# Kernel optimization log

Measured on AMD Instinct MI355X. Metric: run time of the kernel, lower is better.

Reference implementation:

```python
import jax, jax.numpy as jnp
import numpy as np

GROUPS = 2
STRIDE = (1, 1)
PADDING = ((1, 1), (1, 1))
DILATION = (1, 1)


def setup_inputs() -> dict:
    key = jax.random.key(0)
    k1, k2, k3 = jax.random.split(key, 3)
    B, Cin, H, W = 16, 256, 112, 112
    Cout, kH, kW = 256, 3, 3
    x = jax.random.normal(k1, (B, Cin, H, W), dtype=jnp.float32)
    # kaiming_uniform-like scale: fan_in = (Cin/groups)*kH*kW
    fan_in = (Cin // GROUPS) * kH * kW
    bound = float(np.sqrt(1.0 / fan_in))
    weight = jax.random.uniform(k2, (Cout, Cin // GROUPS, kH, kW), dtype=jnp.float32,
                                minval=-bound, maxval=bound)
    bias = jax.random.uniform(k3, (Cout,), dtype=jnp.float32, minval=-bound, maxval=bound)
    return {"x": x, "weight": weight, "bias": bias}


def reference(x, weight, bias):
    # Grouped conv2d: every backend path of SparseGroupedConv2d (sparse triton
    # active-tile kernel, zero-tile skip, dense F.conv2d fallback) computes this
    # exact grouped convolution; the tile machinery only skips zero-energy tiles.
    y = jax.lax.conv_general_dilated(
        x, weight,
        window_strides=STRIDE,
        padding=PADDING,
        rhs_dilation=DILATION,
        dimension_numbers=("NCHW", "OIHW", "NCHW"),
        feature_group_count=GROUPS,
    )
    return y + bias[None, :, None, None]
```

## Files before the change

### kernel.cpp

```cpp
#include <hip/hip_runtime.h>
#include <hip/hip_bf16.h>
#include <stdint.h>

#define BATCH 16
#define CIN   256
#define HH    112
#define WW    112
#define GROUPS 2
#define CG    128
#define COG   128
#define CK    32

typedef __bf16 bf16x8 __attribute__((ext_vector_type(8)));
typedef float  f32x4  __attribute__((ext_vector_type(4)));

#define WB_BYTES   (GROUPS*3*3*COG*CG*2)
#define ZBUF_OFF   WB_BYTES
#define ZBUF_BYTES 8192
#define XB_OFF     (ZBUF_OFF + ZBUF_BYTES)
#define XB_BYTES   ((size_t)BATCH*HH*WW*CIN*2)
#define WS_NEED    ((size_t)XB_OFF + XB_BYTES)

__device__ inline void load_lds16(const void* g, void* l) {
    __builtin_amdgcn_global_load_lds(
        (const __attribute__((address_space(1))) void*)g,
        (__attribute__((address_space(3))) void*)l, 16, 0, 0);
}

__global__ __launch_bounds__(256) void k_wcvt(const float* __restrict__ w,
                                              ushort* __restrict__ wb) {
    int i = blockIdx.x * 256 + threadIdx.x;
    int ci = i & 127;
    int t  = i >> 7;
    int co = t & 127;
    t >>= 7;
    int kw = t % 3; t /= 3;
    int kh = t % 3;
    int g  = t / 3;
    int src = (((g*COG + co)*CG + ci)*3 + kh)*3 + kw;
    __hip_bfloat16 v = __float2bfloat16(w[src]);
    wb[i] = *reinterpret_cast<ushort*>(&v);
}

#define XPAD 113
__global__ __launch_bounds__(256) void k_xcvt(const float* __restrict__ x,
                                              ushort* __restrict__ xb) {
    __shared__ float tile[64 * XPAD];
    int bid = blockIdx.x;
    int cc  = bid & 3;
    int h   = (bid >> 2) % HH;
    int b   = bid / (4 * HH);
    int tid = threadIdx.x;

    const float* src = x + ((size_t)(b*CIN + cc*64) * HH + h) * WW;
    for (int tt = tid; tt < 64*28; tt += 256) {
        int c = tt / 28, v = tt % 28;
        float4 f = *reinterpret_cast<const float4*>(src + (size_t)c*HH*WW + v*4);
        float* d = &tile[c*XPAD + v*4];
        d[0]=f.x; d[1]=f.y; d[2]=f.z; d[3]=f.w;
    }
    __syncthreads();

    if (tid < 224) {
        int w = tid >> 1, half = tid & 1;
        ushort o[32];
#pragma unroll
        for (int j = 0; j < 32; ++j) {
            __hip_bfloat16 v = __float2bfloat16(tile[(half*32 + j)*XPAD + w]);
            o[j] = *reinterpret_cast<ushort*>(&v);
        }
        ushort* dst = xb + (((size_t)(b*HH + h)*WW + w)*CIN + cc*64 + half*32);
        const uint4* o4 = reinterpret_cast<const uint4*>(o);
        uint4* d4 = reinterpret_cast<uint4*>(dst);
        d4[0]=o4[0]; d4[1]=o4[1]; d4[2]=o4[2]; d4[3]=o4[3];
    }
}

__device__ inline void stage_w3(const ushort* __restrict__ wb, ushort* dstbuf,
                                int g, int tap_base, int cin, int wave, int lane) {
    int co = wave*16 + (lane >> 2);
    int ts = (lane & 3) ^ ((lane >> 3) & 3);
#pragma unroll
    for (int i = 0; i < 3; ++i) {
        const ushort* src = wb + (((size_t)(g*9 + tap_base + i)*COG + co)*CG + cin + ts*8);
        load_lds16(src, dstbuf + (i*COG + wave*16)*CK);
    }
}

__device__ inline void xpre48(const ushort* __restrict__ xb, ushort* dstbuf,
                              ushort* dump, const ushort* __restrict__ zbuf,
                              int b, int g, int oh0, int cin, int t, int lane,
                              bool real) {
    if (real && t < 42) {
        int rr = t / 7, ii = t % 7;
        int h  = oh0 - 1 + rr;
        int qv = lane >> 2;
        int w_in = ii*16 + qv;
        int ts = (lane & 3) ^ (((2*rr + 1 + qv) >> 1) & 3);
        const ushort* src = (h >= 0 && h < HH)
            ? xb + (((size_t)(b*HH + h)*WW + w_in)*CIN + g*CG + cin + ts*8)
            : zbuf + lane*8;
        load_lds16(src, dstbuf + (rr*114 + 1 + ii*16)*CK);
    } else {
        load_lds16(zbuf + lane*8, dump);
    }
}

#define WAITV(N) asm volatile("s_waitcnt vmcnt(" #N ")" ::: "memory");

#define TAPX(KH, KW, NT, NC)                                                \
  {                                                                         \
    int sB = lk ^ (((2*(wr + (KH)) + l15 + (KW)) >> 1) & 3);                \
    const ushort* bbase = xcur + ((wr + (KH))*114 + l15 + (KW))*CK + sB*8;  \
    bf16x8 xf[7];                                                           \
    _Pragma("unroll")                                                       \
    for (int i = 0; i < 7; ++i)                                             \
      xf[i] = *reinterpret_cast<const bf16x8*>(bbase + i*16*CK);            \
    const ushort* abase = wcur + ((KW)*COG + wm*64 + l15)*CK + sA*8;        \
    bf16x8 wf[4];                                                           \
    _Pragma("unroll")                                                       \
    for (int u = 0; u < 4; ++u)                                             \
      wf[u] = *reinterpret_cast<const bf16x8*>(abase + u*16*CK);            \
    if ((KW) == 0) stage_w3(wb, wnxt, g, (NT), (NC), wave, lane);           \
    if ((KW) <= 1)                                                          \
      xpre48(xb, xnxt, dump, zbuf, b, g, oh0, cinN,                         \
             wave + 8*((KH)*2 + (KW)), lane, c < 3);                        \
    __builtin_amdgcn_s_barrier();                                           \
    __builtin_amdgcn_s_setprio(1);                                          \
    _Pragma("unroll")                                                       \
    for (int u = 0; u < 4; ++u)                                             \
      _Pragma("unroll")                                                     \
      for (int i = 0; i < 7; ++i)                                           \
        acc[i][u] = __builtin_amdgcn_mfma_f32_16x16x32_bf16(                \
            xf[i], wf[u], acc[i][u], 0, 0, 0);                              \
    __builtin_amdgcn_s_setprio(0);                                          \
    if ((KW) == 2) { if ((KH) == 2) { WAITV(0) } else { WAITV(2) } }        \
    __builtin_amdgcn_s_barrier();                                           \
  }

#define GROUPSEC(KH, NT, NC) TAPX(KH,0,NT,NC) TAPX(KH,1,NT,NC) TAPX(KH,2,NT,NC)

__global__ __launch_bounds__(512, 2) void k_conv(const ushort* __restrict__ xb,
                                                 const ushort* __restrict__ wb,
                                                 const float* __restrict__ bias,
                                                 float* __restrict__ out,
                                                 const ushort* __restrict__ zbuf) {
    __shared__ __align__(16) ushort xs[2][6*114*CK];
    __shared__ __align__(16) ushort wsb[2][3*COG*CK];
    __shared__ __align__(16) ushort dump[512];

    int orig = (blockIdx.x & 7) * 112 + (blockIdx.x >> 3);
    int g   = orig / 448;
    int r   = orig % 448;
    int b   = r / 28;
    int q   = r % 28;
    int oh0 = q * 4;

    int tid  = threadIdx.x;
    int wave = tid >> 6;
    int lane = tid & 63;
    int wm   = wave >> 2;
    int wr   = wave & 3;
    int l15  = lane & 15;
    int lk   = lane >> 4;
    int sA   = lk ^ ((l15 >> 1) & 3);

    for (int t = tid; t < 768; t += 512) {
        int buf = t / 384, r2 = t % 384;
        int rr = r2 / 64, wc = (r2 >> 5) & 1, ch = r2 & 31;
        xs[buf][(rr*114 + wc*113)*CK + ch] = 0;
    }

    float bvreg[4];
#pragma unroll
    for (int u = 0; u < 4; ++u)
        bvreg[u] = bias[g*COG + wm*64 + u*16 + l15];

    f32x4 acc[7][4];
#pragma unroll
    for (int i = 0; i < 7; ++i)
#pragma unroll
        for (int u = 0; u < 4; ++u) acc[i][u] = f32x4{0.f,0.f,0.f,0.f};

    for (int k2 = 0; k2 < 6; ++k2)
        xpre48(xb, xs[0], dump, zbuf, b, g, oh0, 0, wave + 8*k2, lane, true);
    stage_w3(wb, wsb[0], g, 0, 0, wave, lane);
    WAITV(0)
    __builtin_amdgcn_s_barrier();

#pragma unroll 1
    for (int c = 0; c < 4; ++c) {
        const ushort* xcur = xs[c & 1];
        ushort* xnxt = xs[(c & 1) ^ 1];
        int cin  = c * CK;
        int cinN = ((c + 1) & 3) * CK;
        (void)cin;

        {
            const ushort* wcur = wsb[c & 1];
            ushort* wnxt = wsb[(c & 1) ^ 1];
            GROUPSEC(0, 3, c*CK)
        }
        {
            const ushort* wcur = wsb[(c + 1) & 1];
            ushort* wnxt = wsb[c & 1];
            GROUPSEC(1, 6, c*CK)
        }
        {
            const ushort* wcur = wsb[c & 1];
            ushort* wnxt = wsb[(c + 1) & 1];
            GROUPSEC(2, 0, cinN)
        }
    }

    int oh = oh0 + wr;
#pragma unroll
    for (int u = 0; u < 4; ++u) {
        int co = g*COG + wm*64 + u*16 + l15;
        float bv = bvreg[u];
        float* obase = out + (((size_t)(b*CIN + co)*HH + oh)*WW + lk*4);
#pragma unroll
        for (int i = 0; i < 7; ++i) {
            f32x4 v;
            v[0] = acc[i][u][0] + bv;
            v[1] = acc[i][u][1] + bv;
            v[2] = acc[i][u][2] + bv;
            v[3] = acc[i][u][3] + bv;
            *reinterpret_cast<f32x4*>(obase + i*16) = v;
        }
    }
}

__global__ __launch_bounds__(128) void k_direct(const float* __restrict__ x,
                                                const float* __restrict__ w,
                                                const float* __restrict__ bias,
                                                float* __restrict__ out) {
    int bid = blockIdx.x;
    int oh  = bid % HH;
    int t   = bid / HH;
    int co  = t % CIN;
    int b   = t / CIN;
    int ow  = threadIdx.x;
    if (ow >= WW) return;
    int g = co / COG;
    float s = bias[co];
    const float* wp = w + (size_t)co*CG*9;
    const float* xp = x + ((size_t)b*CIN + g*CG)*HH*WW;
    for (int ci = 0; ci < CG; ++ci) {
        const float* xr = xp + (size_t)ci*HH*WW;
        const float* wr_ = wp + ci*9;
#pragma unroll
        for (int kh = 0; kh < 3; ++kh) {
            int ih = oh + kh - 1;
            if (ih < 0 || ih >= HH) continue;
#pragma unroll
            for (int kw = 0; kw < 3; ++kw) {
                int iw = ow + kw - 1;
                if (iw < 0 || iw >= WW) continue;
                s += xr[ih*WW + iw] * wr_[kh*3 + kw];
            }
        }
    }
    out[(((size_t)b*CIN + co)*HH + oh)*WW + ow] = s;
}

extern "C" void kernel_launch(void* const* d_in, const int* in_sizes, int n_in,
                              void* d_out, int out_size, void* d_ws, size_t ws_size,
                              hipStream_t stream) {
    const float* x    = (const float*)d_in[0];
    const float* w    = (const float*)d_in[1];
    const float* bias = (const float*)d_in[2];
    float* out        = (float*)d_out;

    if (ws_size >= WS_NEED) {
        ushort* wb   = (ushort*)d_ws;
        ushort* zb   = (ushort*)((char*)d_ws + ZBUF_OFF);
        ushort* xbuf = (ushort*)((char*)d_ws + XB_OFF);
        hipMemsetAsync(zb, 0, ZBUF_BYTES, stream);
        k_wcvt<<<1152, 256, 0, stream>>>(w, wb);
        k_xcvt<<<BATCH*HH*4, 256, 0, stream>>>(x, xbuf);
        k_conv<<<896, 512, 0, stream>>>(xbuf, wb, bias, out, zb);
    } else {
        k_direct<<<BATCH*CIN*HH, 128, 0, stream>>>(x, w, bias, out);
    }
}
```

Baseline: 235.2 us.

## Load input fragments directly from global into registers, drop LDS input staging

Input activations are no longer staged through LDS. Each wave loads its bf16x8 input fragments straight from global memory into registers, using a larger zero buffer for padding, and alternates two register sets so the loads for the next tap overlap the MFMAs of the current one. Weights for all nine taps are now double-buffered in LDS per channel chunk, which removes most per-tap barriers and leaves one barrier per chunk. The cost is that every wave issues its own uncoalesced global reads with overlap across taps, and register pressure rises with two 7-element fragment sets.

```diff
diff --git a/kernel.cpp b/kernel.cpp
--- a/kernel.cpp
+++ b/kernel.cpp
@@ -16,7 +16,7 @@
 
 #define WB_BYTES   (GROUPS*3*3*COG*CG*2)
 #define ZBUF_OFF   WB_BYTES
-#define ZBUF_BYTES 8192
+#define ZBUF_BYTES 65536
 #define XB_OFF     (ZBUF_OFF + ZBUF_BYTES)
 #define XB_BYTES   ((size_t)BATCH*HH*WW*CIN*2)
 #define WS_NEED    ((size_t)XB_OFF + XB_BYTES)
@@ -87,67 +87,66 @@
     }
 }
 
-__device__ inline void xpre48(const ushort* __restrict__ xb, ushort* dstbuf,
-                              ushort* dump, const ushort* __restrict__ zbuf,
-                              int b, int g, int oh0, int cin, int t, int lane,
-                              bool real) {
-    if (real && t < 42) {
-        int rr = t / 7, ii = t % 7;
-        int h  = oh0 - 1 + rr;
-        int qv = lane >> 2;
-        int w_in = ii*16 + qv;
-        int ts = (lane & 3) ^ (((2*rr + 1 + qv) >> 1) & 3);
-        const ushort* src = (h >= 0 && h < HH)
-            ? xb + (((size_t)(b*HH + h)*WW + w_in)*CIN + g*CG + cin + ts*8)
-            : zbuf + lane*8;
-        load_lds16(src, dstbuf + (rr*114 + 1 + ii*16)*CK);
-    } else {
-        load_lds16(zbuf + lane*8, dump);
-    }
-}
-
-#define WAITV(N) asm volatile("s_waitcnt vmcnt(" #N ")" ::: "memory");
-
-#define TAPX(KH, KW, NT, NC)                                                \
+#define XISSUE(XN, KH2, KW2, CINV)                                          \
   {                                                                         \
-    int sB = lk ^ (((2*(wr + (KH)) + l15 + (KW)) >> 1) & 3);                \
-    const ushort* bbase = xcur + ((wr + (KH))*114 + l15 + (KW))*CK + sB*8;  \
-    bf16x8 xf[7];                                                           \
+    int h_ = oh0 + wr + (KH2) - 1;                                          \
+    const ushort* rowp_ = (h_ >= 0 && h_ < HH)                              \
+        ? xb + ((size_t)(b*HH + h_)*WW)*CIN + coffb + (CINV)                \
+        : zb;                                                               \
     _Pragma("unroll")                                                       \
-    for (int i = 0; i < 7; ++i)                                             \
-      xf[i] = *reinterpret_cast<const bf16x8*>(bbase + i*16*CK);            \
-    const ushort* abase = wcur + ((KW)*COG + wm*64 + l15)*CK + sA*8;        \
-    bf16x8 wf[4];                                                           \
+    for (int n_ = 0; n_ < 7; ++n_) {                                        \
+      const ushort* a_ = rowp_ + (n_*16 + l15 + (KW2) - 1)*CIN;             \
+      if ((KW2) == 0 && n_ == 0) a_ = (l15 == 0)  ? zb + lane*8 : a_;       \
+      if ((KW2) == 2 && n_ == 6) a_ = (l15 == 15) ? zb + lane*8 : a_;       \
+      XN[n_] = *reinterpret_cast<const bf16x8*>(a_);                        \
+    }                                                                       \
+  }
+
+#define WISSUE(WN, WCUR, TAP2)                                              \
+  {                                                                         \
+    const ushort* ab_ = (WCUR) + ((TAP2)*COG + wm*64 + l15)*CK + sA*8;      \
     _Pragma("unroll")                                                       \
-    for (int u = 0; u < 4; ++u)                                             \
-      wf[u] = *reinterpret_cast<const bf16x8*>(abase + u*16*CK);            \
-    if ((KW) == 0) stage_w3(wb, wnxt, g, (NT), (NC), wave, lane);           \
-    if ((KW) <= 1)                                                          \
-      xpre48(xb, xnxt, dump, zbuf, b, g, oh0, cinN,                         \
-             wave + 8*((KH)*2 + (KW)), lane, c < 3);                        \
-    __builtin_amdgcn_s_barrier();                                           \
+    for (int u_ = 0; u_ < 4; ++u_)                                          \
+      WN[u_] = *reinterpret_cast<const bf16x8*>(ab_ + u_*16*CK);            \
+  }
+
+#define MF(XC, WC)                                                          \
+    __builtin_amdgcn_sched_barrier(0);                                      \
     __builtin_amdgcn_s_setprio(1);                                          \
     _Pragma("unroll")                                                       \
-    for (int u = 0; u < 4; ++u)                                             \
+    for (int u_ = 0; u_ < 4; ++u_)                                          \
       _Pragma("unroll")                                                     \
-      for (int i = 0; i < 7; ++i)                                           \
-        acc[i][u] = __builtin_amdgcn_mfma_f32_16x16x32_bf16(                \
-            xf[i], wf[u], acc[i][u], 0, 0, 0);                              \
-    __builtin_amdgcn_s_setprio(0);                                          \
-    if ((KW) == 2) { if ((KH) == 2) { WAITV(0) } else { WAITV(2) } }        \
+      for (int i_ = 0; i_ < 7; ++i_)                                        \
+        acc[i_][u_] = __builtin_amdgcn_mfma_f32_16x16x32_bf16(              \
+            XC[i_], WC[u_], acc[i_][u_], 0, 0, 0);                          \
+    __builtin_amdgcn_s_setprio(0);
+
+#define CHUNK(XA, XB, CIN_, CINN_, WCUR, WNXT, DONEXT)                      \
+  {                                                                         \
+    WISSUE(wfA, WCUR, 0)                                                    \
+    XISSUE(XB, 0, 1, CIN_) WISSUE(wfB, WCUR, 1)                             \
+      stage_w3(wb, WNXT,             g, 0, CINN_, wave, lane); MF(XA, wfA)  \
+    XISSUE(XA, 0, 2, CIN_) WISSUE(wfA, WCUR, 2)                             \
+      stage_w3(wb, WNXT + 3*COG*CK,  g, 3, CINN_, wave, lane); MF(XB, wfB)  \
+    XISSUE(XB, 1, 0, CIN_) WISSUE(wfB, WCUR, 3)                             \
+      stage_w3(wb, WNXT + 6*COG*CK,  g, 6, CINN_, wave, lane); MF(XA, wfA)  \
+    XISSUE(XA, 1, 1, CIN_) WISSUE(wfA, WCUR, 4) MF(XB, wfB)                 \
+    XISSUE(XB, 1, 2, CIN_) WISSUE(wfB, WCUR, 5) MF(XA, wfA)                 \
+    XISSUE(XA, 2, 0, CIN_) WISSUE(wfA, WCUR, 6) MF(XB, wfB)                 \
+    XISSUE(XB, 2, 1, CIN_) WISSUE(wfB, WCUR, 7) MF(XA, wfA)                 \
+    XISSUE(XA, 2, 2, CIN_) WISSUE(wfA, WCUR, 8) MF(XB, wfB)                 \
+    if (DONEXT) { XISSUE(XB, 0, 0, CINN_) }                                 \
+    MF(XA, wfA)                                                             \
+    asm volatile("s_waitcnt vmcnt(7)" ::: "memory");                        \
     __builtin_amdgcn_s_barrier();                                           \
   }
-
-#define GROUPSEC(KH, NT, NC) TAPX(KH,0,NT,NC) TAPX(KH,1,NT,NC) TAPX(KH,2,NT,NC)
 
 __global__ __launch_bounds__(512, 2) void k_conv(const ushort* __restrict__ xb,
                                                  const ushort* __restrict__ wb,
                                                  const float* __restrict__ bias,
                                                  float* __restrict__ out,
-                                                 const ushort* __restrict__ zbuf) {
-    __shared__ __align__(16) ushort xs[2][6*114*CK];
-    __shared__ __align__(16) ushort wsb[2][3*COG*CK];
-    __shared__ __align__(16) ushort dump[512];
+                                                 const ushort* __restrict__ zb) {
+    __shared__ __align__(16) ushort wsb[2][9*COG*CK];
 
     int orig = (blockIdx.x & 7) * 112 + (blockIdx.x >> 3);
     int g   = orig / 448;
@@ -164,12 +163,7 @@
     int l15  = lane & 15;
     int lk   = lane >> 4;
     int sA   = lk ^ ((l15 >> 1) & 3);
-
-    for (int t = tid; t < 768; t += 512) {
-        int buf = t / 384, r2 = t % 384;
-        int rr = r2 / 64, wc = (r2 >> 5) & 1, ch = r2 & 31;
-        xs[buf][(rr*114 + wc*113)*CK + ch] = 0;
-    }
+    int coffb = g*CG + lk*8;
 
     float bvreg[4];
 #pragma unroll
@@ -182,36 +176,19 @@
 #pragma unroll
         for (int u = 0; u < 4; ++u) acc[i][u] = f32x4{0.f,0.f,0.f,0.f};
 
-    for (int k2 = 0; k2 < 6; ++k2)
-        xpre48(xb, xs[0], dump, zbuf, b, g, oh0, 0, wave + 8*k2, lane, true);
-    stage_w3(wb, wsb[0], g, 0, 0, wave, lane);
-    WAITV(0)
+    bf16x8 xf0[7], xf1[7], wfA[4], wfB[4];
+
+    XISSUE(xf0, 0, 0, 0)
+    stage_w3(wb, wsb[0],             g, 0, 0, wave, lane);
+    stage_w3(wb, wsb[0] + 3*COG*CK,  g, 3, 0, wave, lane);
+    stage_w3(wb, wsb[0] + 6*COG*CK,  g, 6, 0, wave, lane);
+    asm volatile("s_waitcnt vmcnt(0)" ::: "memory");
     __builtin_amdgcn_s_barrier();
 
-#pragma unroll 1
-    for (int c = 0; c < 4; ++c) {
-        const ushort* xcur = xs[c & 1];
-        ushort* xnxt = xs[(c & 1) ^ 1];
-        int cin  = c * CK;
-        int cinN = ((c + 1) & 3) * CK;
-        (void)cin;
-
-        {
-            const ushort* wcur = wsb[c & 1];
-            ushort* wnxt = wsb[(c & 1) ^ 1];
-            GROUPSEC(0, 3, c*CK)
-        }
-        {
-            const ushort* wcur = wsb[(c + 1) & 1];
-            ushort* wnxt = wsb[c & 1];
-            GROUPSEC(1, 6, c*CK)
-        }
-        {
-            const ushort* wcur = wsb[c & 1];
-            ushort* wnxt = wsb[(c + 1) & 1];
-            GROUPSEC(2, 0, cinN)
-        }
-    }
+    CHUNK(xf0, xf1, 0*CK, 1*CK, wsb[0], wsb[1], true)
+    CHUNK(xf1, xf0, 1*CK, 2*CK, wsb[1], wsb[0], true)
+    CHUNK(xf0, xf1, 2*CK, 3*CK, wsb[0], wsb[1], true)
+    CHUNK(xf1, xf0, 3*CK, 0*CK, wsb[1], wsb[0], false)
 
     int oh = oh0 + wr;
 #pragma unroll
```

After: 477.6 us. +103.1%, slower.
